# Optimization experiments

Hardware: AMD Instinct MI355X
Metric: run time of the kernel (lower is better)

## Reference

```python
import jax, jax.numpy as jnp
import numpy as np

N_EMBD = 768
FULL_SIZE = 16 * N_EMBD   # 12288
K = 4 * N_EMBD            # iter_size = 3072 (top-k)
B, T = 8, 1024


def setup_inputs() -> dict:
    key = jax.random.key(0)
    k0, k1, k2, k3, k4 = jax.random.split(key, 5)
    s = lambda fan_in: 1.0 / np.sqrt(fan_in)
    return {
        "x": jax.random.normal(k0, (B, T, N_EMBD), dtype=jnp.float32),
        "w1": jax.random.normal(k1, (N_EMBD // 16, N_EMBD), dtype=jnp.float32) * s(N_EMBD),
        "w2": jax.random.normal(k2, (FULL_SIZE, N_EMBD // 16), dtype=jnp.float32) * s(N_EMBD // 16),
        "w_mfc": jax.random.normal(k3, (FULL_SIZE, N_EMBD), dtype=jnp.float32) * s(N_EMBD),
        "w_proj": jax.random.normal(k4, (N_EMBD, FULL_SIZE), dtype=jnp.float32) * s(FULL_SIZE),
    }


def _topk_mask(ck, k):
    # softmax -> top-k indices -> hard 0/1 mask (scatter of constant 1.0)
    probs = jax.nn.softmax(ck, axis=-1)
    _, idx = jax.lax.top_k(probs, k)            # (B, k)
    b = jnp.arange(probs.shape[0])[:, None]
    return jnp.zeros_like(probs).at[b, idx].set(1.0)


def reference(x, w1, w2, w_mfc, w_proj):
    # control net on sequence-mean pooled features
    pooled = x.mean(axis=1)                                  # (B, D)
    ck = jax.nn.relu(pooled @ w1.T) @ w2.T                   # (B, F)
    mask = _topk_mask(ck, K)                                 # (B, F) hard 0/1
    # DynamicMaskedLinear: bmm(x, (W*mask)^T) == (x @ W^T) * mask (0/1 output mask)
    h = jnp.einsum('btd,fd->btf', x, w_mfc) * mask[:, None, :]
    h = jax.nn.relu(h)
    out = jnp.einsum('btf,ef->bte', h, w_proj)               # (B, T, D)
    return out
```

## Files before the change

### kernel.cpp

```cpp
#include <hip/hip_runtime.h>

#define N_EMBD 768
#define FULL   12288
#define KSEL   3072
#define BATCH  8
#define TLEN   1024
#define HID    48

typedef short bf16x8 __attribute__((ext_vector_type(8)));
typedef float f32x4 __attribute__((ext_vector_type(4)));
typedef unsigned short u16x4 __attribute__((ext_vector_type(4)));
typedef unsigned short u16x8 __attribute__((ext_vector_type(8)));

#define MFMA(a, b, c) __builtin_amdgcn_mfma_f32_16x16x32_bf16((a), (b), (c), 0, 0, 0)
#define GLDS(g, l) __builtin_amdgcn_global_load_lds( \
    (const __attribute__((address_space(1))) void*)(const void*)(g), \
    (__attribute__((address_space(3))) void*)(void*)(l), 16, 0, 0)

__device__ __forceinline__ unsigned short f2bf(float f) {
  unsigned u = __float_as_uint(f);
  u += 0x7fffu + ((u >> 16) & 1u);
  return (unsigned short)(u >> 16);
}
__device__ __forceinline__ float bf2f(unsigned short h) {
  return __uint_as_float(((unsigned)h) << 16);
}

__global__ void split_pool_x(const float* __restrict__ x, unsigned short* __restrict__ xh,
                             float* __restrict__ partial) {
  const int s = blockIdx.x;
  const int b = blockIdx.y;
  const int d = blockIdx.z * 256 + threadIdx.x * 4;
  const float* base = x + ((size_t)(b * TLEN + s * 64)) * N_EMBD + d;
  float4 sum = {0.f, 0.f, 0.f, 0.f};
  for (int t = 0; t < 64; ++t) {
    const float4 v = *(const float4*)(base + (size_t)t * N_EMBD);
    sum.x += v.x; sum.y += v.y; sum.z += v.z; sum.w += v.w;
    u16x4 h;
    h.x = f2bf(v.x); h.y = f2bf(v.y); h.z = f2bf(v.z); h.w = f2bf(v.w);
    *(u16x4*)(xh + ((size_t)(b * TLEN + s * 64 + t)) * N_EMBD + d) = h;
  }
  float* pp = partial + (b * 16 + s) * N_EMBD + d;
  pp[0] = sum.x; pp[1] = sum.y; pp[2] = sum.z; pp[3] = sum.w;
}

__global__ __launch_bounds__(256) void control1_kernel(
    const float* __restrict__ partial, const float* __restrict__ w1, float* __restrict__ hid) {
  __shared__ float w1s[HID][385];
  __shared__ float ps[N_EMBD];
  const int b = blockIdx.x;
  const int tid = threadIdx.x;
  for (int d = tid; d < N_EMBD; d += 256) {
    float sum = 0.f;
    #pragma unroll
    for (int s = 0; s < 16; ++s) sum += partial[(b * 16 + s) * N_EMBD + d];
    ps[d] = sum * (1.f / TLEN);
  }
  float acc = 0.f;
  #pragma unroll
  for (int half = 0; half < 2; ++half) {
    __syncthreads();
    for (int i = tid; i < HID * 384; i += 256) {
      const int r = i / 384, c = i % 384;
      w1s[r][c] = w1[r * N_EMBD + half * 384 + c];
    }
    __syncthreads();
    if (tid < HID) {
      const float* pr = ps + half * 384;
      #pragma unroll 8
      for (int d2 = 0; d2 < 384; ++d2) acc = fmaf(pr[d2], w1s[tid][d2], acc);
    }
  }
  if (tid < HID) hid[b * HID + tid] = fmaxf(acc, 0.f);
}

__global__ void control2_kernel(const float* __restrict__ hid, const float* __restrict__ w2,
                                float* __restrict__ ck) {
  const int b = blockIdx.y;
  const int f = blockIdx.x * 256 + threadIdx.x;
  __shared__ float hid_s[HID];
  if (threadIdx.x < HID) hid_s[threadIdx.x] = hid[b * HID + threadIdx.x];
  __syncthreads();
  const float* wr = w2 + (size_t)f * HID;
  float acc = 0.f;
  #pragma unroll
  for (int j = 0; j < HID; ++j) acc = fmaf(hid_s[j], wr[j], acc);
  ck[b * FULL + f] = acc;
}

__global__ void topk_kernel(const float* __restrict__ ck, int* __restrict__ sel) {
  const int b = blockIdx.x;
  const int tid = threadIdx.x;
  const int lane = tid & 63, wv = tid >> 6;
  unsigned key[48];
  const int f_lo = tid * 48;
  #pragma unroll
  for (int i = 0; i < 48; ++i) {
    unsigned u = __float_as_uint(ck[b * FULL + f_lo + i]);
    key[i] = (u & 0x80000000u) ? ~u : (u | 0x80000000u);
  }
  __shared__ unsigned redw[4];
  __shared__ int sg[257], se[257];
  unsigned prefix = 0;
  int remaining = KSEL;
  for (int bit = 31; bit >= 0; --bit) {
    const unsigned want = prefix | (1u << bit);
    const unsigned shifted = want >> bit;
    int cnt = 0;
    #pragma unroll
    for (int i = 0; i < 48; ++i) cnt += ((key[i] >> bit) == shifted) ? 1 : 0;
    #pragma unroll
    for (int off = 1; off < 64; off <<= 1) cnt += __shfl_xor(cnt, off, 64);
    if (lane == 0) redw[wv] = (unsigned)cnt;
    __syncthreads();
    const int c = (int)(redw[0] + redw[1] + redw[2] + redw[3]);
    __syncthreads();
    if (c >= remaining) prefix = want;
    else remaining -= c;
  }
  const unsigned kth = prefix;
  int cg = 0, ce = 0;
  #pragma unroll
  for (int i = 0; i < 48; ++i) { cg += (key[i] > kth) ? 1 : 0; ce += (key[i] == kth) ? 1 : 0; }
  sg[tid] = cg; se[tid] = ce;
  __syncthreads();
  if (tid == 0) {
    int ag = 0, ae = 0;
    for (int i = 0; i < 256; ++i) {
      int tg = sg[i], te = se[i];
      sg[i] = ag; se[i] = ae;
      ag += tg; ae += te;
    }
    sg[256] = ag;
  }
  __syncthreads();
  const int ng = sg[256];
  int gpos = sg[tid], epos = se[tid];
  #pragma unroll
  for (int i = 0; i < 48; ++i) {
    const unsigned k = key[i];
    const int f = f_lo + i;
    if (k > kth) {
      sel[b * KSEL + (gpos++)] = f;
    } else if (k == kth) {
      const int p = ng + epos;
      if (p < KSEL) sel[b * KSEL + p] = f;
      ++epos;
    }
  }
}

__global__ void round_w_kernel(const float* __restrict__ src, unsigned short* __restrict__ dst, int n4) {
  const int idx = blockIdx.x * 256 + threadIdx.x;
  if (idx >= n4) return;
  const float4 v = ((const float4*)src)[idx];
  u16x4 h;
  h.x = f2bf(v.x); h.y = f2bf(v.y); h.z = f2bf(v.z); h.w = f2bf(v.w);
  ((u16x4*)dst)[idx] = h;
}

__global__ __launch_bounds__(256) void gather_wp_kernel(
    const float* __restrict__ wproj, const int* __restrict__ sel,
    unsigned short* __restrict__ wph) {
  __shared__ unsigned short row_s[FULL];
  const int e = blockIdx.x;
  const int tid = threadIdx.x;
  const float* wr = wproj + (size_t)e * FULL;
  #pragma unroll
  for (int i = 0; i < FULL / 4 / 256; ++i) {
    const int idx = tid + i * 256;
    const float4 v = ((const float4*)wr)[idx];
    u16x4 h;
    h.x = f2bf(v.x); h.y = f2bf(v.y); h.z = f2bf(v.z); h.w = f2bf(v.w);
    *(u16x4*)(row_s + idx * 4) = h;
  }
  __syncthreads();
  #pragma unroll
  for (int i = 0; i < 12; ++i) {
    const int idx = tid + i * 256;
    const int b = idx / 384, c = idx % 384;
    const int* sp = sel + b * KSEL + c * 8;
    const int4 s0 = ((const int4*)sp)[0];
    const int4 s1 = ((const int4*)sp)[1];
    u16x8 v;
    v[0] = row_s[s0.x]; v[1] = row_s[s0.y]; v[2] = row_s[s0.z]; v[3] = row_s[s0.w];
    v[4] = row_s[s1.x]; v[5] = row_s[s1.y]; v[6] = row_s[s1.z]; v[7] = row_s[s1.w];
    *(u16x8*)(wph + ((size_t)(b * N_EMBD + e)) * KSEL + c * 8) = v;
  }
}

__global__ __launch_bounds__(256) void gemm1_mfma(
    const unsigned short* __restrict__ xh, const unsigned short* __restrict__ wh,
    const int* __restrict__ sel, unsigned short* __restrict__ hh) {
  __shared__ __align__(16) char sm[49152];
  const int nx = TLEN / 128, ny = KSEL / 128;
  const int nwg = nx * ny * BATCH;
  int lin = blockIdx.x + nx * (blockIdx.y + ny * blockIdx.z);
  int swz = (lin & 7) * (nwg >> 3) + (lin >> 3);
  const int bx = swz % nx; int tmp = swz / nx;
  const int by = tmp % ny; const int b = tmp / ny;
  const int t0 = bx * 128, f0 = by * 128;

  const int tid = threadIdx.x;
  const int wv = tid >> 6, lane = tid & 63;
  const int srow = tid >> 2, sslot = tid & 3;
  const int wb = wv * 1024;

  const char* pxh = (const char*)xh;
  const char* pwh = (const char*)wh;
  const size_t aoff  = ((size_t)(b * TLEN + t0 + srow)) * 1536 + sslot * 16;
  const size_t aoff2 = aoff + (size_t)64 * 1536;
  const int* selb = sel + b * KSEL;
  const size_t boff  = (size_t)selb[f0 + srow] * 1536 + sslot * 16;
  const size_t boff2 = (size_t)selb[f0 + srow + 64] * 1536 + sslot * 16;

  const int fr = lane & 15, kg = lane >> 4;
  const int fo = fr * 64 + kg * 16;
  const int m0 = (wv >> 1) * 64, n0 = (wv & 1) * 64;

  f32x4 acc[4][4];
  const f32x4 z4 = {0.f, 0.f, 0.f, 0.f};
  #pragma unroll
  for (int mi = 0; mi < 4; ++mi)
    #pragma unroll
    for (int ni = 0; ni < 4; ++ni) acc[mi][ni] = z4;

  auto stage = [&](int bo, int kb) {
    GLDS(pxh + aoff  + kb, sm + bo + 0     + wb);
    GLDS(pxh + aoff2 + kb, sm + bo + 4096  + wb);
    GLDS(pwh + boff  + kb, sm + bo + 8192  + wb);
    GLDS(pwh + boff2 + kb, sm + bo + 12288 + wb);
  };
  const int NIT = N_EMBD * 2 / 64;
  stage(0, 0);
  stage(16384, 64);
  for (int it = 0; it < NIT; ++it) {
    if (it < NIT - 1) asm volatile("s_waitcnt vmcnt(4)" ::: "memory");
    else              asm volatile("s_waitcnt vmcnt(0)" ::: "memory");
    __builtin_amdgcn_s_barrier();
    __builtin_amdgcn_sched_barrier(0);
    const int cur = (it % 3) << 14;
    if (it + 2 < NIT) stage(((it + 2) % 3) << 14, (it + 2) * 64);
    bf16x8 ah[4], bh[4];
    #pragma unroll
    for (int i = 0; i < 4; ++i) {
      ah[i] = *(const bf16x8*)(sm + cur + 0    + (m0 + i * 16) * 64 + fo);
      bh[i] = *(const bf16x8*)(sm + cur + 8192 + (n0 + i * 16) * 64 + fo);
    }
    #pragma unroll
    for (int mi = 0; mi < 4; ++mi)
      #pragma unroll
      for (int ni = 0; ni < 4; ++ni)
        acc[mi][ni] = MFMA(ah[mi], bh[ni], acc[mi][ni]);
  }
  __syncthreads();
  unsigned short* lh = (unsigned short*)sm;
  const int rowg = lane >> 4, colc = lane & 15;
  #pragma unroll
  for (int mi = 0; mi < 4; ++mi)
    #pragma unroll
    for (int ni = 0; ni < 4; ++ni) {
      const int row = m0 + mi * 16 + rowg * 4;
      const int col = n0 + ni * 16 + colc;
      #pragma unroll
      for (int j = 0; j < 4; ++j)
        lh[(row + j) * 128 + col] = f2bf(fmaxf(acc[mi][ni][j], 0.f));
    }
  __syncthreads();
  const int orow = tid >> 4, oc = tid & 15;
  #pragma unroll
  for (int i2 = 0; i2 < 8; ++i2) {
    const int row = orow + i2 * 16;
    const u16x8 v = *(const u16x8*)&lh[row * 128 + oc * 8];
    *(u16x8*)(hh + ((size_t)(b * TLEN + t0 + row)) * KSEL + f0 + oc * 8) = v;
  }
}

__global__ __launch_bounds__(256) void gemm2_mfma(
    const unsigned short* __restrict__ hh, const unsigned short* __restrict__ wph,
    float* __restrict__ out) {
  __shared__ __align__(16) char sm[73728];
  const int lin = blockIdx.x;
  const int b = lin & 7;
  const int j = lin >> 3;
  const int bx = j & 7, by = j >> 3;
  const int t0 = bx * 128, e0 = by * 64;

  const int tid = threadIdx.x;
  const int wv = tid >> 6, lane = tid & 63;
  const int wb = wv * 1024;

  const char* pa = (const char*)hh;
  const char* pb = (const char*)wph;
  const size_t aoff  = ((size_t)(b * TLEN + t0 + (tid >> 2))) * 6144 + (tid & 3) * 16;
  const size_t aoff2 = aoff + (size_t)64 * 6144;
  const size_t boff  = ((size_t)(b * N_EMBD + e0 + (tid >> 2))) * 6144 + (tid & 3) * 16;

  const int fr = lane & 15, kg = lane >> 4;
  const int fo = fr * 64 + kg * 16;
  const int m0 = (wv >> 1) * 64, n0 = (wv & 1) * 32;

  f32x4 acc[4][2];
  const f32x4 z4 = {0.f, 0.f, 0.f, 0.f};
  #pragma unroll
  for (int mi = 0; mi < 4; ++mi)
    #pragma unroll
    for (int ni = 0; ni < 2; ++ni) acc[mi][ni] = z4;

  auto stage = [&](int bo, int d) {
    GLDS(pa + aoff  + d,      sm + bo + 0     + wb);
    GLDS(pa + aoff2 + d,      sm + bo + 4096  + wb);
    GLDS(pa + aoff  + d + 64, sm + bo + 8192  + wb);
    GLDS(pa + aoff2 + d + 64, sm + bo + 12288 + wb);
    GLDS(pb + boff  + d,      sm + bo + 16384 + wb);
    GLDS(pb + boff  + d + 64, sm + bo + 20480 + wb);
  };
  const int NIT = KSEL * 2 / 128;
  stage(0, 0);
  stage(24576, 128);
  for (int it = 0; it < NIT; ++it) {
    if (it < NIT - 1) asm volatile("s_waitcnt vmcnt(6)" ::: "memory");
    else              asm volatile("s_waitcnt vmcnt(0)" ::: "memory");
    __builtin_amdgcn_s_barrier();
    __builtin_amdgcn_sched_barrier(0);
    const int cur = (it % 3) * 24576;
    if (it + 2 < NIT) stage(((it + 2) % 3) * 24576, (it + 2) * 128);
    bf16x8 ah[4][2], bh[2][2];
    #pragma unroll
    for (int i = 0; i < 4; ++i) {
      const int ra = (m0 + i * 16) * 64 + fo;
      ah[i][0] = *(const bf16x8*)(sm + cur + 0    + ra);
      ah[i][1] = *(const bf16x8*)(sm + cur + 8192 + ra);
    }
    #pragma unroll
    for (int i = 0; i < 2; ++i) {
      const int rb = (n0 + i * 16) * 64 + fo;
      bh[i][0] = *(const bf16x8*)(sm + cur + 16384 + rb);
      bh[i][1] = *(const bf16x8*)(sm + cur + 20480 + rb);
    }
    #pragma unroll
    for (int c = 0; c < 2; ++c)
      #pragma unroll
      for (int mi = 0; mi < 4; ++mi)
        #pragma unroll
        for (int ni = 0; ni < 2; ++ni)
          acc[mi][ni] = MFMA(ah[mi][c], bh[ni][c], acc[mi][ni]);
  }
  const int rowg = lane >> 4, colc = lane & 15;
  #pragma unroll
  for (int mi = 0; mi < 4; ++mi)
    #pragma unroll
    for (int ni = 0; ni < 2; ++ni) {
      const int m = t0 + m0 + mi * 16 + rowg * 4;
      const int e = e0 + n0 + ni * 16 + colc;
      const size_t base = ((size_t)(b * TLEN + m)) * N_EMBD + e;
      #pragma unroll
      for (int jj = 0; jj < 4; ++jj)
        out[base + (size_t)jj * N_EMBD] = acc[mi][ni][jj];
    }
}

extern "C" void kernel_launch(void* const* d_in, const int* in_sizes, int n_in,
                              void* d_out, int out_size, void* d_ws, size_t ws_size,
                              hipStream_t stream) {
  const float* x      = (const float*)d_in[0];
  const float* w1     = (const float*)d_in[1];
  const float* w2     = (const float*)d_in[2];
  const float* w_mfc  = (const float*)d_in[3];
  const float* w_proj = (const float*)d_in[4];
  float* out = (float*)d_out;

  char* ws = (char*)d_ws;
  size_t off = 0;
  auto alloc = [&](size_t bytes) -> void* {
    void* p = ws + off;
    off += (bytes + 255) & ~(size_t)255;
    return p;
  };
  const size_t NX  = (size_t)BATCH * TLEN * N_EMBD;
  const size_t NW  = (size_t)FULL * N_EMBD;
  const size_t NWP = (size_t)BATCH * N_EMBD * KSEL;
  const size_t NH  = (size_t)BATCH * TLEN * KSEL;

  float* partial = (float*)alloc((size_t)BATCH * 16 * N_EMBD * 4);
  float* hid     = (float*)alloc((size_t)BATCH * HID * 4);
  float* ckbuf   = (float*)alloc((size_t)BATCH * FULL * 4);
  int*   sel     = (int*)  alloc((size_t)BATCH * KSEL * 4);
  unsigned short* xh  = (unsigned short*)alloc(NX * 2);
  unsigned short* wh  = (unsigned short*)alloc(NW * 2);
  unsigned short* wph = (unsigned short*)alloc(NWP * 2);
  unsigned short* hh  = (unsigned short*)alloc(NH * 2);

  split_pool_x<<<dim3(16, BATCH, 3), 64, 0, stream>>>(x, xh, partial);
  round_w_kernel<<<(int)(NW / 4 / 256), 256, 0, stream>>>(w_mfc, wh, (int)(NW / 4));
  control1_kernel<<<BATCH, 256, 0, stream>>>(partial, w1, hid);
  control2_kernel<<<dim3(FULL / 256, BATCH), 256, 0, stream>>>(hid, w2, ckbuf);
  topk_kernel<<<BATCH, 256, 0, stream>>>(ckbuf, sel);
  gather_wp_kernel<<<768, 256, 0, stream>>>(w_proj, sel, wph);
  gemm1_mfma<<<dim3(TLEN / 128, KSEL / 128, BATCH), 256, 0, stream>>>(xh, wh, sel, hh);
  gemm2_mfma<<<768, 256, 0, stream>>>(hh, wph, out);
}
```

Before: 323.4 us.

## Fuse x pooling and weight rounding into one prep kernel; halve gemm2 K-step

Merges the x split/pool/bf16 conversion and the w_mfc bf16 rounding into one launch. Blocks 0-127 handle x and the remaining 576 blocks convert the weights, so one launch is dropped and the two independent streaming jobs can overlap. Separately, gemm2 now uses a 32-wide K step per stage instead of 64. This shrinks shared memory from 72KB to 36KB, which may allow more blocks per CU, at the cost of twice as many barrier-synchronized iterations.

```diff
diff --git a/kernel.cpp b/kernel.cpp
--- a/kernel.cpp
+++ b/kernel.cpp
@@ -26,22 +26,38 @@
   return __uint_as_float(((unsigned)h) << 16);
 }
 
-__global__ void split_pool_x(const float* __restrict__ x, unsigned short* __restrict__ xh,
-                             float* __restrict__ partial) {
-  const int s = blockIdx.x;
-  const int b = blockIdx.y;
-  const int d = blockIdx.z * 256 + threadIdx.x * 4;
-  const float* base = x + ((size_t)(b * TLEN + s * 64)) * N_EMBD + d;
-  float4 sum = {0.f, 0.f, 0.f, 0.f};
-  for (int t = 0; t < 64; ++t) {
-    const float4 v = *(const float4*)(base + (size_t)t * N_EMBD);
-    sum.x += v.x; sum.y += v.y; sum.z += v.z; sum.w += v.w;
-    u16x4 h;
-    h.x = f2bf(v.x); h.y = f2bf(v.y); h.z = f2bf(v.z); h.w = f2bf(v.w);
-    *(u16x4*)(xh + ((size_t)(b * TLEN + s * 64 + t)) * N_EMBD + d) = h;
-  }
-  float* pp = partial + (b * 16 + s) * N_EMBD + d;
-  pp[0] = sum.x; pp[1] = sum.y; pp[2] = sum.z; pp[3] = sum.w;
+__global__ __launch_bounds__(256) void prep_kernel(
+    const float* __restrict__ x, unsigned short* __restrict__ xh, float* __restrict__ partial,
+    const float* __restrict__ w_mfc, unsigned short* __restrict__ wh) {
+  if (blockIdx.x < 128) {
+    const int s = blockIdx.x & 15;
+    const int b = blockIdx.x >> 4;
+    const int tid = threadIdx.x;
+    if (tid < 192) {
+      const int d = tid * 4;
+      const float* base = x + ((size_t)(b * TLEN + s * 64)) * N_EMBD + d;
+      float4 sum = {0.f, 0.f, 0.f, 0.f};
+      for (int t = 0; t < 64; ++t) {
+        const float4 v = *(const float4*)(base + (size_t)t * N_EMBD);
+        sum.x += v.x; sum.y += v.y; sum.z += v.z; sum.w += v.w;
+        u16x4 h;
+        h.x = f2bf(v.x); h.y = f2bf(v.y); h.z = f2bf(v.z); h.w = f2bf(v.w);
+        *(u16x4*)(xh + ((size_t)(b * TLEN + s * 64 + t)) * N_EMBD + d) = h;
+      }
+      float* pp = partial + (b * 16 + s) * N_EMBD + d;
+      pp[0] = sum.x; pp[1] = sum.y; pp[2] = sum.z; pp[3] = sum.w;
+    }
+  } else {
+    const int blk = blockIdx.x - 128;
+    #pragma unroll
+    for (int i = 0; i < 16; ++i) {
+      const int idx = (blk * 16 + i) * 256 + threadIdx.x;
+      const float4 v = ((const float4*)w_mfc)[idx];
+      u16x4 h;
+      h.x = f2bf(v.x); h.y = f2bf(v.y); h.z = f2bf(v.z); h.w = f2bf(v.w);
+      ((u16x4*)wh)[idx] = h;
+    }
+  }
 }
 
 __global__ __launch_bounds__(256) void control1_kernel(
@@ -148,15 +164,6 @@
       ++epos;
     }
   }
-}
-
-__global__ void round_w_kernel(const float* __restrict__ src, unsigned short* __restrict__ dst, int n4) {
-  const int idx = blockIdx.x * 256 + threadIdx.x;
-  if (idx >= n4) return;
-  const float4 v = ((const float4*)src)[idx];
-  u16x4 h;
-  h.x = f2bf(v.x); h.y = f2bf(v.y); h.z = f2bf(v.z); h.w = f2bf(v.w);
-  ((u16x4*)dst)[idx] = h;
 }
 
 __global__ __launch_bounds__(256) void gather_wp_kernel(
@@ -279,7 +286,7 @@
 __global__ __launch_bounds__(256) void gemm2_mfma(
     const unsigned short* __restrict__ hh, const unsigned short* __restrict__ wph,
     float* __restrict__ out) {
-  __shared__ __align__(16) char sm[73728];
+  __shared__ __align__(16) char sm[36864];
   const int lin = blockIdx.x;
   const int b = lin & 7;
   const int j = lin >> 3;
@@ -308,43 +315,32 @@
     for (int ni = 0; ni < 2; ++ni) acc[mi][ni] = z4;
 
   auto stage = [&](int bo, int d) {
-    GLDS(pa + aoff  + d,      sm + bo + 0     + wb);
-    GLDS(pa + aoff2 + d,      sm + bo + 4096  + wb);
-    GLDS(pa + aoff  + d + 64, sm + bo + 8192  + wb);
-    GLDS(pa + aoff2 + d + 64, sm + bo + 12288 + wb);
-    GLDS(pb + boff  + d,      sm + bo + 16384 + wb);
-    GLDS(pb + boff  + d + 64, sm + bo + 20480 + wb);
+    GLDS(pa + aoff  + d, sm + bo + 0    + wb);
+    GLDS(pa + aoff2 + d, sm + bo + 4096 + wb);
+    GLDS(pb + boff  + d, sm + bo + 8192 + wb);
   };
-  const int NIT = KSEL * 2 / 128;
+  const int NIT = KSEL / 32;
   stage(0, 0);
-  stage(24576, 128);
+  stage(12288, 64);
   for (int it = 0; it < NIT; ++it) {
-    if (it < NIT - 1) asm volatile("s_waitcnt vmcnt(6)" ::: "memory");
+    if (it < NIT - 1) asm volatile("s_waitcnt vmcnt(3)" ::: "memory");
     else              asm volatile("s_waitcnt vmcnt(0)" ::: "memory");
     __builtin_amdgcn_s_barrier();
     __builtin_amdgcn_sched_barrier(0);
-    const int cur = (it % 3) * 24576;
-    if (it + 2 < NIT) stage(((it + 2) % 3) * 24576, (it + 2) * 128);
-    bf16x8 ah[4][2], bh[2][2];
-    #pragma unroll
-    for (int i = 0; i < 4; ++i) {
-      const int ra = (m0 + i * 16) * 64 + fo;
-      ah[i][0] = *(const bf16x8*)(sm + cur + 0    + ra);
-      ah[i][1] = *(const bf16x8*)(sm + cur + 8192 + ra);
-    }
-    #pragma unroll
-    for (int i = 0; i < 2; ++i) {
-      const int rb = (n0 + i * 16) * 64 + fo;
-      bh[i][0] = *(const bf16x8*)(sm + cur + 16384 + rb);
-      bh[i][1] = *(const bf16x8*)(sm + cur + 20480 + rb);
-    }
-    #pragma unroll
-    for (int c = 0; c < 2; ++c)
+    const int cur = (it % 3) * 12288;
+    if (it + 2 < NIT) stage(((it + 2) % 3) * 12288, (it + 2) * 64);
+    bf16x8 ah[4], bh[2];
+    #pragma unroll
+    for (int i = 0; i < 4; ++i)
+      ah[i] = *(const bf16x8*)(sm + cur + 0    + (m0 + i * 16) * 64 + fo);
+    #pragma unroll
+    for (int i = 0; i < 2; ++i)
+      bh[i] = *(const bf16x8*)(sm + cur + 8192 + (n0 + i * 16) * 64 + fo);
+    #pragma unroll
+    for (int mi = 0; mi < 4; ++mi)
       #pragma unroll
-      for (int mi = 0; mi < 4; ++mi)
-        #pragma unroll
-        for (int ni = 0; ni < 2; ++ni)
-          acc[mi][ni] = MFMA(ah[mi][c], bh[ni][c], acc[mi][ni]);
+      for (int ni = 0; ni < 2; ++ni)
+        acc[mi][ni] = MFMA(ah[mi], bh[ni], acc[mi][ni]);
   }
   const int rowg = lane >> 4, colc = lane & 15;
   #pragma unroll
@@ -391,8 +387,7 @@
   unsigned short* wph = (unsigned short*)alloc(NWP * 2);
   unsigned short* hh  = (unsigned short*)alloc(NH * 2);
 
-  split_pool_x<<<dim3(16, BATCH, 3), 64, 0, stream>>>(x, xh, partial);
-  round_w_kernel<<<(int)(NW / 4 / 256), 256, 0, stream>>>(w_mfc, wh, (int)(NW / 4));
+  prep_kernel<<<704, 256, 0, stream>>>(x, xh, partial, w_mfc, wh);
   control1_kernel<<<BATCH, 256, 0, stream>>>(partial, w1, hid);
   control2_kernel<<<dim3(FULL / 256, BATCH), 256, 0, stream>>>(hid, w2, ckbuf);
   topk_kernel<<<BATCH, 256, 0, stream>>>(ckbuf, sel);
```

New measurement: 321.3 us. No clear change (-0.7%).
